# Kernel optimization log

Measured on AMD Instinct MI355X. Metric: run time of the kernel, lower is better.

## Reference

```python
import jax, jax.numpy as jnp
import numpy as np

NUM_NODES = 100000
NUM_EDGES = 400000
F_IN = 16          # num_node_features
F_EDGE = 8         # num_edge_features
EMB = 16           # emb_size
NUM_GRAPHS = 256


def setup_inputs() -> dict:
    key = jax.random.key(0)
    ks = jax.random.split(key, 12)
    x = jax.random.normal(ks[0], (NUM_NODES, F_IN), dtype=jnp.float32)
    edge_index = jax.random.randint(ks[1], (2, NUM_EDGES), 0, NUM_NODES, dtype=jnp.int32)
    edge_attr = jax.random.normal(ks[2], (NUM_EDGES, F_EDGE), dtype=jnp.float32)
    batch = jnp.sort(jax.random.randint(ks[3], (NUM_NODES,), 0, NUM_GRAPHS, dtype=jnp.int32))
    s = 0.1
    # edge-network MLP: Linear(F_EDGE -> F_IN*EMB) + ReLU (torch Linear convention: W[out,in])
    nn1_w = jax.random.normal(ks[4], (F_IN * EMB, F_EDGE), dtype=jnp.float32) * s
    nn1_b = jax.random.normal(ks[5], (F_IN * EMB,), dtype=jnp.float32) * s
    # NNConv root weight (bias=False Linear) + separate bias
    root_w = jax.random.normal(ks[6], (EMB, F_IN), dtype=jnp.float32) * s
    conv_b = jax.random.normal(ks[7], (EMB,), dtype=jnp.float32) * s
    lin1_w = jax.random.normal(ks[8], (EMB, 2 * EMB), dtype=jnp.float32) * s
    lin1_b = jax.random.normal(ks[9], (EMB,), dtype=jnp.float32) * s
    lin2_w = jax.random.normal(ks[10], (1, EMB), dtype=jnp.float32) * s
    lin2_b = jax.random.normal(ks[11], (1,), dtype=jnp.float32) * s
    return {"x": x, "edge_index": edge_index, "edge_attr": edge_attr, "batch": batch,
            "nn1_w": nn1_w, "nn1_b": nn1_b, "root_w": root_w, "conv_b": conv_b,
            "lin1_w": lin1_w, "lin1_b": lin1_b, "lin2_w": lin2_w, "lin2_b": lin2_b}


def reference(x, edge_index, edge_attr, batch, nn1_w, nn1_b, root_w, conv_b,
              lin1_w, lin1_b, lin2_w, lin2_b):
    N = x.shape[0]
    src, dst = edge_index[0], edge_index[1]  # PyG: message flows src(j) -> dst(i)
    # edge network -> per-edge weight matrices [E, F_IN, EMB]
    w = jax.nn.relu(edge_attr @ nn1_w.T + nn1_b).reshape(-1, F_IN, EMB)
    # gather source features, per-edge matmul
    msg = jnp.einsum('ei,eio->eo', x[src], w)  # [E, EMB]
    # scatter-mean into target nodes
    sums = jax.ops.segment_sum(msg, dst, num_segments=N)
    cnt = jax.ops.segment_sum(jnp.ones((msg.shape[0],), msg.dtype), dst, num_segments=N)
    agg = sums / jnp.maximum(cnt, 1.0)[:, None]
    # NNConv: root transform + aggregated messages + bias, then outer ReLU
    h = jax.nn.relu(agg + x @ root_w.T + conv_b)  # [N, EMB]
    # global max pool and global mean pool per graph
    gmax = jax.ops.segment_max(h, batch, num_segments=NUM_GRAPHS)
    gsum = jax.ops.segment_sum(h, batch, num_segments=NUM_GRAPHS)
    gcnt = jax.ops.segment_sum(jnp.ones((N,), h.dtype), batch, num_segments=NUM_GRAPHS)
    gmean = gsum / jnp.maximum(gcnt, 1.0)[:, None]
    pooled = jnp.concatenate([gmax, gmean], axis=1)  # [G, 2*EMB]
    h2 = jax.nn.relu(pooled @ lin1_w.T + lin1_b)
    out = h2 @ lin2_w.T + lin2_b  # [G, 1]
    return out
```

## Files before the change

kernel.cpp:

```cpp
#include <hip/hip_runtime.h>

#define NUM_NODES 100000
#define NUM_EDGES 400000
#define F_IN 16
#define F_EDGE 8
#define EMB 16
#define NUM_GRAPHS 256

#define EDGE_TILES 5
#define EDGE_BLOCKS (NUM_EDGES / (32 * EDGE_TILES))

#define NPB 128
#define NODE_BLOCKS ((NUM_NODES + NPB - 1) / NPB)


__global__ __launch_bounds__(256, 3) void edge_kernel(
    const float* __restrict__ x, const int* __restrict__ ei,
    const float* __restrict__ ea, const float* __restrict__ nn1_w,
    const float* __restrict__ nn1_b, float* __restrict__ sums,
    float* __restrict__ cnt)
{
    __shared__ float wtp[256 * 12];
    __shared__ float btp[16 * 20];

    const int tid = threadIdx.x;
    const int eL  = tid >> 4;
    const int o   = tid & 15;
    const int eb0 = blockIdx.x * EDGE_TILES * 32;

    int srcA[EDGE_TILES], srcB[EDGE_TILES];
    #pragma unroll
    for (int t = 0; t < EDGE_TILES; t++) {
        srcA[t] = ei[eb0 + t * 32 + eL];
        srcB[t] = ei[eb0 + t * 32 + 16 + eL];
    }
    __builtin_amdgcn_sched_barrier(0);

    {
        const float4 w0 = *(const float4*)&nn1_w[tid * 8];
        const float4 w1 = *(const float4*)&nn1_w[tid * 8 + 4];
        *(float4*)&wtp[tid * 12]     = w0;
        *(float4*)&wtp[tid * 12 + 4] = w1;
    }
    btp[(tid & 15) * 20 + (tid >> 4)] = nn1_b[tid];
    __syncthreads();

    float br[F_IN];
    #pragma unroll
    for (int r = 0; r < 4; r++) {
        const float4 b4 = *(const float4*)&btp[o * 20 + 4 * r];
        br[4 * r + 0] = b4.x; br[4 * r + 1] = b4.y;
        br[4 * r + 2] = b4.z; br[4 * r + 3] = b4.w;
    }

    float4 pA00, pA01, pA10, pA11; float pX0[16], pX1[16]; int pDA, pDB;
    float4 qA00, qA01, qA10, qA11; float qX0[16], qX1[16]; int qDA, qDB;

#define LOAD_TILE(T, A00, A01, A10, A11, X0, X1, DA, DB) do {               \
        const int eA_ = eb0 + (T) * 32 + eL;                                \
        const int eB_ = eA_ + 16;                                           \
        DA = ei[NUM_EDGES + eA_];                                           \
        DB = ei[NUM_EDGES + eB_];                                           \
        A00 = *(const float4*)&ea[eA_ * 8];                                 \
        A01 = *(const float4*)&ea[eA_ * 8 + 4];                             \
        A10 = *(const float4*)&ea[eB_ * 8];                                 \
        A11 = *(const float4*)&ea[eB_ * 8 + 4];                             \
        _Pragma("unroll")                                                   \
        for (int r = 0; r < 4; r++) {                                       \
            const float4 v0 = *(const float4*)&x[srcA[T] * 16 + 4 * r];     \
            const float4 v1 = *(const float4*)&x[srcB[T] * 16 + 4 * r];     \
            X0[4*r+0] = v0.x; X0[4*r+1] = v0.y;                             \
            X0[4*r+2] = v0.z; X0[4*r+3] = v0.w;                             \
            X1[4*r+0] = v1.x; X1[4*r+1] = v1.y;                             \
            X1[4*r+2] = v1.z; X1[4*r+3] = v1.w;                             \
        }                                                                   \
    } while (0)

#define COMPUTE_TILE(A00, A01, A10, A11, X0, X1, DA, DB) do {               \
        float acc0 = 0.f, acc1 = 0.f;                                       \
        _Pragma("unroll")                                                   \
        for (int i = 0; i < F_IN; i++) {                                    \
            const float* wr = &wtp[(i * 16 + o) * 12];                      \
            const float4 w0 = *(const float4*)wr;                           \
            const float4 w1 = *(const float4*)(wr + 4);                     \
            float u = br[i];                                                \
            u = fmaf(A00.x, w0.x, u); u = fmaf(A00.y, w0.y, u);             \
            u = fmaf(A00.z, w0.z, u); u = fmaf(A00.w, w0.w, u);             \
            u = fmaf(A01.x, w1.x, u); u = fmaf(A01.y, w1.y, u);             \
            u = fmaf(A01.z, w1.z, u); u = fmaf(A01.w, w1.w, u);             \
            acc0 = fmaf(X0[i], fmaxf(u, 0.f), acc0);                        \
            float v = br[i];                                                \
            v = fmaf(A10.x, w0.x, v); v = fmaf(A10.y, w0.y, v);             \
            v = fmaf(A10.z, w0.z, v); v = fmaf(A10.w, w0.w, v);             \
            v = fmaf(A11.x, w1.x, v); v = fmaf(A11.y, w1.y, v);             \
            v = fmaf(A11.w, w1.w, v); v = fmaf(A11.z, w1.z, v);             \
            acc1 = fmaf(X1[i], fmaxf(v, 0.f), acc1);                        \
        }                                                                   \
        atomicAdd(&sums[DA * 16 + o], acc0);                                \
        atomicAdd(&sums[DB * 16 + o], acc1);                                \
        if (o == 0) {                                                       \
            atomicAdd(&cnt[DA], 1.f);                                       \
            atomicAdd(&cnt[DB], 1.f);                                       \
        }                                                                   \
    } while (0)

    LOAD_TILE(0, pA00, pA01, pA10, pA11, pX0, pX1, pDA, pDB);
    #pragma unroll
    for (int t = 0; t < EDGE_TILES; t++) {
        if ((t & 1) == 0) {
            if (t + 1 < EDGE_TILES)
                LOAD_TILE(t + 1, qA00, qA01, qA10, qA11, qX0, qX1, qDA, qDB);
            __builtin_amdgcn_sched_barrier(0);
            COMPUTE_TILE(pA00, pA01, pA10, pA11, pX0, pX1, pDA, pDB);
        } else {
            if (t + 1 < EDGE_TILES)
                LOAD_TILE(t + 1, pA00, pA01, pA10, pA11, pX0, pX1, pDA, pDB);
            __builtin_amdgcn_sched_barrier(0);
            COMPUTE_TILE(qA00, qA01, qA10, qA11, qX0, qX1, qDA, qDB);
        }
    }
#undef LOAD_TILE
#undef COMPUTE_TILE
}

__global__ __launch_bounds__(256) void node_kernel(
    const float* __restrict__ x, const int* __restrict__ batch,
    const float* __restrict__ root_w, const float* __restrict__ conv_b,
    const float* __restrict__ sums, const float* __restrict__ cnt,
    unsigned int* __restrict__ gmax, float* __restrict__ gsum,
    float* __restrict__ gcnt)
{
    __shared__ float rwT[256];
    __shared__ float xsh[256];
    __shared__ float ssh[256];
    __shared__ float csh[16];
    __shared__ int   bsh[16];
    __shared__ float hsh[256];

    const int tid = threadIdx.x;
    const int j   = tid >> 4;
    const int o   = tid & 15;
    const int n0  = blockIdx.x * NPB;

    rwT[(tid & 15) * 16 + (tid >> 4)] = root_w[tid];
    const float cb = conv_b[o];

    int   curg = batch[n0];
    float am = 0.f, asum = 0.f, ac = 0.f;

    for (int s0 = 0; s0 < NPB; s0 += 16) {
        const int base = n0 + s0;
        const int idx  = base * 16 + tid;
        const bool v   = (idx < NUM_NODES * 16);
        const float xv = v ? x[idx]    : 0.f;
        const float sv = v ? sums[idx] : 0.f;
        float cv = 1.f; int bv = -1;
        if (tid < 16) {
            const int n = base + tid;
            if (n < NUM_NODES) { cv = cnt[n]; bv = batch[n]; }
        }
        __syncthreads();
        xsh[tid] = xv; ssh[tid] = sv;
        if (tid < 16) { csh[tid] = cv; bsh[tid] = bv; }
        __syncthreads();

        float a = cb + ssh[j * 16 + o] / fmaxf(csh[j], 1.f);
        #pragma unroll
        for (int i = 0; i < F_IN; i++)
            a = fmaf(xsh[j * 16 + i], rwT[i * 16 + o], a);
        hsh[tid] = fmaxf(a, 0.f);
        __syncthreads();

        if (tid < 16) {
            #pragma unroll 1
            for (int jj = 0; jj < 16; jj++) {
                const int g = bsh[jj];
                if (g < 0) break;
                if (g != curg) {
                    atomicMax(&gmax[curg * 16 + o], __float_as_uint(am));
                    atomicAdd(&gsum[curg * 16 + o], asum);
                    if (o == 0) atomicAdd(&gcnt[curg], ac);
                    am = 0.f; asum = 0.f; ac = 0.f; curg = g;
                }
                const float h = hsh[jj * 16 + o];
                am = fmaxf(am, h); asum += h; ac += 1.f;
            }
        }
    }

    if (tid < 16) {
        atomicMax(&gmax[curg * 16 + o], __float_as_uint(am));
        atomicAdd(&gsum[curg * 16 + o], asum);
        if (o == 0) atomicAdd(&gcnt[curg], ac);
    }
}

__global__ __launch_bounds__(256) void head_kernel(
    const unsigned int* __restrict__ gmax, const float* __restrict__ gsum,
    const float* __restrict__ gcnt,
    const float* __restrict__ lin1_w, const float* __restrict__ lin1_b,
    const float* __restrict__ lin2_w, const float* __restrict__ lin2_b,
    float* __restrict__ out)
{
    const int g = threadIdx.x;

    float pooled[2 * EMB];
    #pragma unroll
    for (int o = 0; o < EMB; o++) pooled[o] = __uint_as_float(gmax[g * 16 + o]);
    const float c = fmaxf(gcnt[g], 1.f);
    #pragma unroll
    for (int o = 0; o < EMB; o++) pooled[EMB + o] = gsum[g * 16 + o] / c;

    float acc = lin2_b[0];
    #pragma unroll
    for (int k = 0; k < EMB; k++) {
        float a = lin1_b[k];
        #pragma unroll
        for (int cc = 0; cc < 2 * EMB; cc++)
            a = fmaf(pooled[cc], lin1_w[k * 32 + cc], a);
        acc = fmaf(fmaxf(a, 0.f), lin2_w[k], acc);
    }
    out[g] = acc;
}

extern "C" void kernel_launch(void* const* d_in, const int* in_sizes, int n_in,
                              void* d_out, int out_size, void* d_ws, size_t ws_size,
                              hipStream_t stream) {
    const float* x      = (const float*)d_in[0];
    const int*   ei     = (const int*)d_in[1];
    const float* ea     = (const float*)d_in[2];
    const int*   batch  = (const int*)d_in[3];
    const float* nn1_w  = (const float*)d_in[4];
    const float* nn1_b  = (const float*)d_in[5];
    const float* root_w = (const float*)d_in[6];
    const float* conv_b = (const float*)d_in[7];
    const float* lin1_w = (const float*)d_in[8];
    const float* lin1_b = (const float*)d_in[9];
    const float* lin2_w = (const float*)d_in[10];
    const float* lin2_b = (const float*)d_in[11];
    float* out = (float*)d_out;

    float*        sums = (float*)d_ws;
    float*        cnt  = sums + (size_t)NUM_NODES * EMB;
    unsigned int* gmax = (unsigned int*)(cnt + NUM_NODES);
    float*        gsum = (float*)(gmax + NUM_GRAPHS * EMB);
    float*        gcnt = gsum + NUM_GRAPHS * EMB;

    const size_t zero_bytes = sizeof(float) *
        ((size_t)NUM_NODES * EMB + NUM_NODES + 2 * NUM_GRAPHS * EMB + NUM_GRAPHS);
    hipMemsetAsync(d_ws, 0, zero_bytes, stream);

    edge_kernel<<<EDGE_BLOCKS, 256, 0, stream>>>(x, ei, ea, nn1_w, nn1_b, sums, cnt);
    node_kernel<<<NODE_BLOCKS, 256, 0, stream>>>(
        x, batch, root_w, conv_b, sums, cnt, gmax, gsum, gcnt);
    head_kernel<<<1, 256, 0, stream>>>(gmax, gsum, gcnt,
                                       lin1_w, lin1_b, lin2_w, lin2_b, out);
}
```

Before: 163.5 us.

## Hold edge weights in registers and fuse node, pool and head per graph

The edge kernel now gives each thread one output channel across 16 edges and keeps the edge-network weights and bias in registers instead of LDS. Each block covers 10 tiles and runs at 2 waves per EU. The node, pooling and head kernels are merged into one kernel with a block per graph. Each block binary-searches the sorted batch array for its node range and reduces max and mean in-block, which removes the pooling atomics, one launch and part of the memset. The risks are higher register pressure in the edge kernel, and poor load balance and few blocks (256) in the graph kernel.

```diff
diff --git a/kernel.cpp b/kernel.cpp
--- a/kernel.cpp
+++ b/kernel.cpp
@@ -7,220 +7,189 @@
 #define EMB 16
 #define NUM_GRAPHS 256
 
-#define EDGE_TILES 5
-#define EDGE_BLOCKS (NUM_EDGES / (32 * EDGE_TILES))
-
-#define NPB 128
-#define NODE_BLOCKS ((NUM_NODES + NPB - 1) / NPB)
-
-
-__global__ __launch_bounds__(256, 3) void edge_kernel(
+#define ET 10
+#define EDGE_BLOCKS (NUM_EDGES / (16 * ET))
+
+
+__global__ __launch_bounds__(256, 2) void edge_kernel(
     const float* __restrict__ x, const int* __restrict__ ei,
     const float* __restrict__ ea, const float* __restrict__ nn1_w,
     const float* __restrict__ nn1_b, float* __restrict__ sums,
     float* __restrict__ cnt)
 {
-    __shared__ float wtp[256 * 12];
-    __shared__ float btp[16 * 20];
-
     const int tid = threadIdx.x;
-    const int eL  = tid >> 4;
-    const int o   = tid & 15;
-    const int eb0 = blockIdx.x * EDGE_TILES * 32;
-
-    int srcA[EDGE_TILES], srcB[EDGE_TILES];
-    #pragma unroll
-    for (int t = 0; t < EDGE_TILES; t++) {
-        srcA[t] = ei[eb0 + t * 32 + eL];
-        srcB[t] = ei[eb0 + t * 32 + 16 + eL];
-    }
+    const int e   = tid & 15;
+    const int o   = tid >> 4;
+    const int eb0 = blockIdx.x * (16 * ET);
+
+    int srcT[ET];
+    #pragma unroll
+    for (int t = 0; t < ET; t++) srcT[t] = ei[eb0 + t * 16 + e];
     __builtin_amdgcn_sched_barrier(0);
 
-    {
-        const float4 w0 = *(const float4*)&nn1_w[tid * 8];
-        const float4 w1 = *(const float4*)&nn1_w[tid * 8 + 4];
-        *(float4*)&wtp[tid * 12]     = w0;
-        *(float4*)&wtp[tid * 12 + 4] = w1;
-    }
-    btp[(tid & 15) * 20 + (tid >> 4)] = nn1_b[tid];
-    __syncthreads();
-
-    float br[F_IN];
-    #pragma unroll
-    for (int r = 0; r < 4; r++) {
-        const float4 b4 = *(const float4*)&btp[o * 20 + 4 * r];
-        br[4 * r + 0] = b4.x; br[4 * r + 1] = b4.y;
-        br[4 * r + 2] = b4.z; br[4 * r + 3] = b4.w;
-    }
-
-    float4 pA00, pA01, pA10, pA11; float pX0[16], pX1[16]; int pDA, pDB;
-    float4 qA00, qA01, qA10, qA11; float qX0[16], qX1[16]; int qDA, qDB;
-
-#define LOAD_TILE(T, A00, A01, A10, A11, X0, X1, DA, DB) do {               \
-        const int eA_ = eb0 + (T) * 32 + eL;                                \
-        const int eB_ = eA_ + 16;                                           \
-        DA = ei[NUM_EDGES + eA_];                                           \
-        DB = ei[NUM_EDGES + eB_];                                           \
-        A00 = *(const float4*)&ea[eA_ * 8];                                 \
-        A01 = *(const float4*)&ea[eA_ * 8 + 4];                             \
-        A10 = *(const float4*)&ea[eB_ * 8];                                 \
-        A11 = *(const float4*)&ea[eB_ * 8 + 4];                             \
+    float4 w0r[F_IN], w1r[F_IN];
+    float  br[F_IN];
+    #pragma unroll
+    for (int i = 0; i < F_IN; i++) {
+        const float* wp = &nn1_w[(i * 16 + o) * 8];
+        w0r[i] = *(const float4*)wp;
+        w1r[i] = *(const float4*)(wp + 4);
+        br[i]  = nn1_b[i * 16 + o];
+    }
+    __builtin_amdgcn_sched_barrier(0);
+
+#define LOAD_TILE(T, A0, A1, XR, D) do {                                    \
+        const int eI = eb0 + (T) * 16 + e;                                  \
+        D  = ei[NUM_EDGES + eI];                                            \
+        A0 = *(const float4*)&ea[eI * 8];                                   \
+        A1 = *(const float4*)&ea[eI * 8 + 4];                               \
         _Pragma("unroll")                                                   \
         for (int r = 0; r < 4; r++) {                                       \
-            const float4 v0 = *(const float4*)&x[srcA[T] * 16 + 4 * r];     \
-            const float4 v1 = *(const float4*)&x[srcB[T] * 16 + 4 * r];     \
-            X0[4*r+0] = v0.x; X0[4*r+1] = v0.y;                             \
-            X0[4*r+2] = v0.z; X0[4*r+3] = v0.w;                             \
-            X1[4*r+0] = v1.x; X1[4*r+1] = v1.y;                             \
-            X1[4*r+2] = v1.z; X1[4*r+3] = v1.w;                             \
+            const float4 v = *(const float4*)&x[srcT[T] * 16 + 4 * r];      \
+            XR[4*r+0] = v.x; XR[4*r+1] = v.y;                               \
+            XR[4*r+2] = v.z; XR[4*r+3] = v.w;                               \
         }                                                                   \
     } while (0)
 
-#define COMPUTE_TILE(A00, A01, A10, A11, X0, X1, DA, DB) do {               \
-        float acc0 = 0.f, acc1 = 0.f;                                       \
+#define COMPUTE_TILE(A0, A1, XR, D) do {                                    \
+        float acc = 0.f;                                                    \
         _Pragma("unroll")                                                   \
         for (int i = 0; i < F_IN; i++) {                                    \
-            const float* wr = &wtp[(i * 16 + o) * 12];                      \
-            const float4 w0 = *(const float4*)wr;                           \
-            const float4 w1 = *(const float4*)(wr + 4);                     \
             float u = br[i];                                                \
-            u = fmaf(A00.x, w0.x, u); u = fmaf(A00.y, w0.y, u);             \
-            u = fmaf(A00.z, w0.z, u); u = fmaf(A00.w, w0.w, u);             \
-            u = fmaf(A01.x, w1.x, u); u = fmaf(A01.y, w1.y, u);             \
-            u = fmaf(A01.z, w1.z, u); u = fmaf(A01.w, w1.w, u);             \
-            acc0 = fmaf(X0[i], fmaxf(u, 0.f), acc0);                        \
-            float v = br[i];                                                \
-            v = fmaf(A10.x, w0.x, v); v = fmaf(A10.y, w0.y, v);             \
-            v = fmaf(A10.z, w0.z, v); v = fmaf(A10.w, w0.w, v);             \
-            v = fmaf(A11.x, w1.x, v); v = fmaf(A11.y, w1.y, v);             \
-            v = fmaf(A11.w, w1.w, v); v = fmaf(A11.z, w1.z, v);             \
-            acc1 = fmaf(X1[i], fmaxf(v, 0.f), acc1);                        \
+            u = fmaf(A0.x, w0r[i].x, u); u = fmaf(A0.y, w0r[i].y, u);       \
+            u = fmaf(A0.z, w0r[i].z, u); u = fmaf(A0.w, w0r[i].w, u);       \
+            u = fmaf(A1.x, w1r[i].x, u); u = fmaf(A1.y, w1r[i].y, u);       \
+            u = fmaf(A1.z, w1r[i].z, u); u = fmaf(A1.w, w1r[i].w, u);       \
+            acc = fmaf(XR[i], fmaxf(u, 0.f), acc);                          \
         }                                                                   \
-        atomicAdd(&sums[DA * 16 + o], acc0);                                \
-        atomicAdd(&sums[DB * 16 + o], acc1);                                \
-        if (o == 0) {                                                       \
-            atomicAdd(&cnt[DA], 1.f);                                       \
-            atomicAdd(&cnt[DB], 1.f);                                       \
-        }                                                                   \
+        atomicAdd(&sums[D * 16 + o], acc);                                  \
+        if (o == 0) atomicAdd(&cnt[D], 1.f);                                \
     } while (0)
 
-    LOAD_TILE(0, pA00, pA01, pA10, pA11, pX0, pX1, pDA, pDB);
-    #pragma unroll
-    for (int t = 0; t < EDGE_TILES; t++) {
+    float4 pA0, pA1; float pX[F_IN]; int pD;
+    float4 qA0, qA1; float qX[F_IN]; int qD;
+
+    LOAD_TILE(0, pA0, pA1, pX, pD);
+    #pragma unroll
+    for (int t = 0; t < ET; t++) {
         if ((t & 1) == 0) {
-            if (t + 1 < EDGE_TILES)
-                LOAD_TILE(t + 1, qA00, qA01, qA10, qA11, qX0, qX1, qDA, qDB);
+            if (t + 1 < ET) LOAD_TILE(t + 1, qA0, qA1, qX, qD);
             __builtin_amdgcn_sched_barrier(0);
-            COMPUTE_TILE(pA00, pA01, pA10, pA11, pX0, pX1, pDA, pDB);
+            COMPUTE_TILE(pA0, pA1, pX, pD);
         } else {
-            if (t + 1 < EDGE_TILES)
-                LOAD_TILE(t + 1, pA00, pA01, pA10, pA11, pX0, pX1, pDA, pDB);
+            if (t + 1 < ET) LOAD_TILE(t + 1, pA0, pA1, pX, pD);
             __builtin_amdgcn_sched_barrier(0);
-            COMPUTE_TILE(qA00, qA01, qA10, qA11, qX0, qX1, qDA, qDB);
+            COMPUTE_TILE(qA0, qA1, qX, qD);
         }
     }
 #undef LOAD_TILE
 #undef COMPUTE_TILE
 }
 
-__global__ __launch_bounds__(256) void node_kernel(
+__global__ __launch_bounds__(256) void graph_kernel(
     const float* __restrict__ x, const int* __restrict__ batch,
     const float* __restrict__ root_w, const float* __restrict__ conv_b,
     const float* __restrict__ sums, const float* __restrict__ cnt,
-    unsigned int* __restrict__ gmax, float* __restrict__ gsum,
-    float* __restrict__ gcnt)
-{
-    __shared__ float rwT[256];
-    __shared__ float xsh[256];
-    __shared__ float ssh[256];
-    __shared__ float csh[16];
-    __shared__ int   bsh[16];
-    __shared__ float hsh[256];
-
-    const int tid = threadIdx.x;
-    const int j   = tid >> 4;
-    const int o   = tid & 15;
-    const int n0  = blockIdx.x * NPB;
-
-    rwT[(tid & 15) * 16 + (tid >> 4)] = root_w[tid];
-    const float cb = conv_b[o];
-
-    int   curg = batch[n0];
-    float am = 0.f, asum = 0.f, ac = 0.f;
-
-    for (int s0 = 0; s0 < NPB; s0 += 16) {
-        const int base = n0 + s0;
-        const int idx  = base * 16 + tid;
-        const bool v   = (idx < NUM_NODES * 16);
-        const float xv = v ? x[idx]    : 0.f;
-        const float sv = v ? sums[idx] : 0.f;
-        float cv = 1.f; int bv = -1;
-        if (tid < 16) {
-            const int n = base + tid;
-            if (n < NUM_NODES) { cv = cnt[n]; bv = batch[n]; }
-        }
-        __syncthreads();
-        xsh[tid] = xv; ssh[tid] = sv;
-        if (tid < 16) { csh[tid] = cv; bsh[tid] = bv; }
-        __syncthreads();
-
-        float a = cb + ssh[j * 16 + o] / fmaxf(csh[j], 1.f);
-        #pragma unroll
-        for (int i = 0; i < F_IN; i++)
-            a = fmaf(xsh[j * 16 + i], rwT[i * 16 + o], a);
-        hsh[tid] = fmaxf(a, 0.f);
-        __syncthreads();
-
-        if (tid < 16) {
-            #pragma unroll 1
-            for (int jj = 0; jj < 16; jj++) {
-                const int g = bsh[jj];
-                if (g < 0) break;
-                if (g != curg) {
-                    atomicMax(&gmax[curg * 16 + o], __float_as_uint(am));
-                    atomicAdd(&gsum[curg * 16 + o], asum);
-                    if (o == 0) atomicAdd(&gcnt[curg], ac);
-                    am = 0.f; asum = 0.f; ac = 0.f; curg = g;
-                }
-                const float h = hsh[jj * 16 + o];
-                am = fmaxf(am, h); asum += h; ac += 1.f;
-            }
-        }
-    }
-
-    if (tid < 16) {
-        atomicMax(&gmax[curg * 16 + o], __float_as_uint(am));
-        atomicAdd(&gsum[curg * 16 + o], asum);
-        if (o == 0) atomicAdd(&gcnt[curg], ac);
-    }
-}
-
-__global__ __launch_bounds__(256) void head_kernel(
-    const unsigned int* __restrict__ gmax, const float* __restrict__ gsum,
-    const float* __restrict__ gcnt,
     const float* __restrict__ lin1_w, const float* __restrict__ lin1_b,
     const float* __restrict__ lin2_w, const float* __restrict__ lin2_b,
     float* __restrict__ out)
 {
-    const int g = threadIdx.x;
-
-    float pooled[2 * EMB];
-    #pragma unroll
-    for (int o = 0; o < EMB; o++) pooled[o] = __uint_as_float(gmax[g * 16 + o]);
-    const float c = fmaxf(gcnt[g], 1.f);
-    #pragma unroll
-    for (int o = 0; o < EMB; o++) pooled[EMB + o] = gsum[g * 16 + o] / c;
-
-    float acc = lin2_b[0];
-    #pragma unroll
-    for (int k = 0; k < EMB; k++) {
+    __shared__ float redM[4][16];
+    __shared__ float redS[4][16];
+
+    const int g   = blockIdx.x;
+    const int tid = threadIdx.x;
+    const int j   = tid >> 4;
+    const int o   = tid & 15;
+    const int jw  = j & 3;
+
+    float rwr[F_IN];
+    #pragma unroll
+    for (int r = 0; r < 4; r++) {
+        const float4 v = *(const float4*)&root_w[o * 16 + 4 * r];
+        rwr[4*r+0] = v.x; rwr[4*r+1] = v.y; rwr[4*r+2] = v.z; rwr[4*r+3] = v.w;
+    }
+    const float cb = conv_b[o];
+
+    int lo0 = 0, hi0 = NUM_NODES, lo1 = 0, hi1 = NUM_NODES;
+    while (lo0 < hi0 || lo1 < hi1) {
+        const int m0 = (lo0 + hi0) >> 1;
+        const int m1 = (lo1 + hi1) >> 1;
+        int b0 = 0, b1 = 0;
+        if (lo0 < hi0) b0 = batch[m0];
+        if (lo1 < hi1) b1 = batch[m1];
+        if (lo0 < hi0) { if (b0 < g)     lo0 = m0 + 1; else hi0 = m0; }
+        if (lo1 < hi1) { if (b1 < g + 1) lo1 = m1 + 1; else hi1 = m1; }
+    }
+    const int start = lo0, end = lo1;
+
+    float am = 0.f, asum = 0.f;
+
+    int base = start;
+    float xv = 0.f, sv = 0.f, cv = 1.f;
+    if (base < end) {
+        const int n = base + j;
+        const bool v = n < end;
+        xv = v ? x[n * 16 + o]    : 0.f;
+        sv = v ? sums[n * 16 + o] : 0.f;
+        cv = v ? cnt[n]           : 1.f;
+    }
+    while (base < end) {
+        const int nbase = base + 16;
+        float xv1 = 0.f, sv1 = 0.f, cv1 = 1.f;
+        if (nbase < end) {
+            const int n1 = nbase + j;
+            const bool v1 = n1 < end;
+            xv1 = v1 ? x[n1 * 16 + o]    : 0.f;
+            sv1 = v1 ? sums[n1 * 16 + o] : 0.f;
+            cv1 = v1 ? cnt[n1]           : 1.f;
+        }
+        __builtin_amdgcn_sched_barrier(0);
+
+        float a = cb + sv / fmaxf(cv, 1.f);
+        #pragma unroll
+        for (int i = 0; i < F_IN; i++)
+            a = fmaf(__shfl(xv, (jw << 4) | i, 64), rwr[i], a);
+        const bool v = (base + j) < end;
+        const float h = v ? fmaxf(a, 0.f) : 0.f;
+        am = fmaxf(am, h);
+        asum += h;
+
+        xv = xv1; sv = sv1; cv = cv1;
+        base = nbase;
+    }
+
+    am   = fmaxf(am, __shfl_xor(am, 16, 64));
+    am   = fmaxf(am, __shfl_xor(am, 32, 64));
+    asum = asum + __shfl_xor(asum, 16, 64);
+    asum = asum + __shfl_xor(asum, 32, 64);
+    const int w = tid >> 6;
+    if ((tid & 63) < 16) { redM[w][o] = am; redS[w][o] = asum; }
+    __syncthreads();
+
+    if (tid < 64) {
+        const int k = tid & 15;
+        const float amF = fmaxf(fmaxf(redM[0][k], redM[1][k]),
+                                fmaxf(redM[2][k], redM[3][k]));
+        const float asF = (redS[0][k] + redS[1][k]) + (redS[2][k] + redS[3][k]);
+        const float c   = fmaxf((float)(end - start), 1.f);
+        const float mnF = asF / c;
+
         float a = lin1_b[k];
         #pragma unroll
-        for (int cc = 0; cc < 2 * EMB; cc++)
-            a = fmaf(pooled[cc], lin1_w[k * 32 + cc], a);
-        acc = fmaf(fmaxf(a, 0.f), lin2_w[k], acc);
-    }
-    out[g] = acc;
+        for (int cc = 0; cc < 16; cc++)
+            a = fmaf(__shfl(amF, cc, 64), lin1_w[k * 32 + cc], a);
+        #pragma unroll
+        for (int cc = 0; cc < 16; cc++)
+            a = fmaf(__shfl(mnF, cc, 64), lin1_w[k * 32 + 16 + cc], a);
+        const float ra = fmaxf(a, 0.f);
+
+        float acc = lin2_b[0];
+        #pragma unroll
+        for (int k2 = 0; k2 < 16; k2++)
+            acc = fmaf(__shfl(ra, k2, 64), lin2_w[k2], acc);
+        if (tid == 0) out[g] = acc;
+    }
 }
 
 extern "C" void kernel_launch(void* const* d_in, const int* in_sizes, int n_in,
@@ -240,19 +209,14 @@
     const float* lin2_b = (const float*)d_in[11];
     float* out = (float*)d_out;
 
-    float*        sums = (float*)d_ws;
-    float*        cnt  = sums + (size_t)NUM_NODES * EMB;
-    unsigned int* gmax = (unsigned int*)(cnt + NUM_NODES);
-    float*        gsum = (float*)(gmax + NUM_GRAPHS * EMB);
-    float*        gcnt = gsum + NUM_GRAPHS * EMB;
-
-    const size_t zero_bytes = sizeof(float) *
-        ((size_t)NUM_NODES * EMB + NUM_NODES + 2 * NUM_GRAPHS * EMB + NUM_GRAPHS);
+    float* sums = (float*)d_ws;
+    float* cnt  = sums + (size_t)NUM_NODES * EMB;
+
+    const size_t zero_bytes = sizeof(float) * ((size_t)NUM_NODES * EMB + NUM_NODES);
     hipMemsetAsync(d_ws, 0, zero_bytes, stream);
 
     edge_kernel<<<EDGE_BLOCKS, 256, 0, stream>>>(x, ei, ea, nn1_w, nn1_b, sums, cnt);
-    node_kernel<<<NODE_BLOCKS, 256, 0, stream>>>(
-        x, batch, root_w, conv_b, sums, cnt, gmax, gsum, gcnt);
-    head_kernel<<<1, 256, 0, stream>>>(gmax, gsum, gcnt,
-                                       lin1_w, lin1_b, lin2_w, lin2_b, out);
+    graph_kernel<<<NUM_GRAPHS, 256, 0, stream>>>(
+        x, batch, root_w, conv_b, sums, cnt,
+        lin1_w, lin1_b, lin2_w, lin2_b, out);
 }
```

Result: slower. 215.6 us (+31.8%).
